# Performance work log

Hardware: AMD Instinct MI355X
Metric: run time of the kernel (lower is better)

The kernel has to match this reference:

```python
import jax, jax.numpy as jnp
import numpy as np

B, N, CT, CS, CP, H, NB = 1, 1024, 768, 384, 16, 16, 4
DH = CT // H
NL, NK = 8, 32          # n_local_tokens, n_keys
K = NL + NK
SCALE = 1.0 / np.sqrt(DH)


def _ln(x, g=None, b=None, eps=1e-5):
    m = jnp.mean(x, -1, keepdims=True)
    v = jnp.var(x, -1, keepdims=True)
    y = (x - m) * jax.lax.rsqrt(v + eps)
    if g is not None:
        y = y * g
    if b is not None:
        y = y + b
    return y


def _adaln(a, s, sln_g, sw, sb, shw):
    # AF3 AdaLN: a <- sigmoid(Lin(s_n)) * LN(a) + LinNoBias(s_n)
    an = _ln(a)
    sn = _ln(s, sln_g)
    return jax.nn.sigmoid(sn @ sw + sb) * an + sn @ shw


def _indices(X_L):
    # n_local sequence neighbours (clamped window) + n_keys spatial nearest
    off = jnp.arange(NL) - NL // 2
    loc = jnp.clip(jnp.arange(N)[:, None] + off[None, :], 0, N - 1)  # [N,NL]
    d2 = jnp.sum((X_L[:, :, None, :] - X_L[:, None, :, :]) ** 2, -1)  # [B,N,N]
    _, nk = jax.lax.top_k(-d2, NK)                                    # [B,N,NK]
    loc = jnp.broadcast_to(loc[None], (X_L.shape[0], N, NL))
    return jnp.concatenate([loc, nk], -1)                             # [B,N,K]


def setup_inputs() -> dict:
    key = jax.random.key(0)
    ks = list(jax.random.split(key, 24))
    f32 = jnp.float32

    def rn(k, shape, s=0.02):
        return (jax.random.normal(k, shape) * s).astype(f32)

    d = {}
    d['A_I'] = jax.random.normal(ks[0], (B, N, CT), f32)
    d['S_I'] = jax.random.normal(ks[1], (B, N, CS), f32)
    d['Z_II'] = jax.random.normal(ks[2], (B, N, N, CP), f32)
    d['X_L'] = jax.random.normal(ks[3], (B, N, 3), f32) * 10.0
    d['f'] = jax.random.randint(ks[4], (B, N), 0, 4)
    # attention-pair-bias block params (stacked over NB blocks)
    d['aln1_sln_g'] = jnp.ones((NB, CS), f32)
    d['aln1_sw'] = rn(ks[5], (NB, CS, CT))
    d['aln1_sb'] = jnp.zeros((NB, CT), f32)
    d['aln1_shw'] = rn(ks[6], (NB, CS, CT))
    d['Wq'] = rn(ks[7], (NB, CT, CT))
    d['bq'] = jnp.zeros((NB, CT), f32)
    d['Wk'] = rn(ks[8], (NB, CT, CT))
    d['Wv'] = rn(ks[9], (NB, CT, CT))
    d['pair_ln_g'] = jnp.ones((NB, CP), f32)
    d['pair_ln_b'] = jnp.zeros((NB, CP), f32)
    d['Wb'] = rn(ks[10], (NB, CP, H))
    d['Wg'] = rn(ks[11], (NB, CT, CT))
    d['Wo'] = rn(ks[12], (NB, CT, CT))
    d['sg_w'] = rn(ks[13], (NB, CS, CT))
    d['sg_b'] = jnp.full((NB, CT), -2.0, f32)   # LinearBiasInit(-2.0)
    # conditioned transition block params
    d['aln2_sln_g'] = jnp.ones((NB, CS), f32)
    d['aln2_sw'] = rn(ks[14], (NB, CS, CT))
    d['aln2_sb'] = jnp.zeros((NB, CT), f32)
    d['aln2_shw'] = rn(ks[15], (NB, CS, CT))
    d['t_w1'] = rn(ks[16], (NB, CT, 2 * CT))
    d['t_w2'] = rn(ks[17], (NB, CT, 2 * CT))
    d['t_w3'] = rn(ks[18], (NB, 2 * CT, CT))
    d['tsg_w'] = rn(ks[19], (NB, CS, CT))
    d['tsg_b'] = jnp.full((NB, CT), -2.0, f32)
    return d


def reference(A_I, S_I, Z_II, X_L, f,
              aln1_sln_g, aln1_sw, aln1_sb, aln1_shw,
              Wq, bq, Wk, Wv, pair_ln_g, pair_ln_b, Wb, Wg, Wo, sg_w, sg_b,
              aln2_sln_g, aln2_sw, aln2_sb, aln2_shw,
              t_w1, t_w2, t_w3, tsg_w, tsg_b):
    idx = _indices(X_L)                       # [B,N,K] int
    bb = jnp.arange(B)[:, None, None]
    nn_ = jnp.arange(N)[None, :, None]
    zg = Z_II[bb, nn_, idx]                   # [B,N,K,CP] gathered pair reps
    A = A_I
    for i in range(NB):
        # LocalAttentionPairBias
        an = _adaln(A, S_I, aln1_sln_g[i], aln1_sw[i], aln1_sb[i], aln1_shw[i])
        q = (an @ Wq[i] + bq[i]).reshape(B, N, H, DH)
        kg = (an @ Wk[i])[bb, idx].reshape(B, N, K, H, DH)
        vg = (an @ Wv[i])[bb, idx].reshape(B, N, K, H, DH)
        bias = _ln(zg, pair_ln_g[i], pair_ln_b[i]) @ Wb[i]      # [B,N,K,H]
        sc = jnp.einsum('bnhd,bnkhd->bnhk', q, kg) * SCALE + jnp.swapaxes(bias, -1, -2)
        w = jax.nn.softmax(sc, -1)                               # [B,N,H,K]
        o = jnp.einsum('bnhk,bnkhd->bnhd', w, vg).reshape(B, N, CT)
        o = jax.nn.sigmoid(an @ Wg[i]) * o                       # per-channel gate
        o = jax.nn.sigmoid(S_I @ sg_w[i] + sg_b[i]) * (o @ Wo[i])
        A = A + o                                                # dropout=0 (eval)
        # ConditionedTransitionBlock (SwiGLU, n=2)
        an2 = _adaln(A, S_I, aln2_sln_g[i], aln2_sw[i], aln2_sb[i], aln2_shw[i])
        hb = jax.nn.silu(an2 @ t_w1[i]) * (an2 @ t_w2[i])
        A = A + jax.nn.sigmoid(S_I @ tsg_w[i] + tsg_b[i]) * (hb @ t_w3[i])
    return A
```

## Files before the change

### kernel.cpp

```cpp
#include <hip/hip_runtime.h>
#include <hip/hip_bf16.h>
#include <math.h>
#include <stdint.h>

#define NTOK 1024
#define CT   768
#define CS   384
#define CP   16
#define NH   16
#define DH   48
#define NBLK 4
#define NL   8
#define NKEY 32
#define KTOT 40
#define SCALE_ 0.14433756729740643f

#define WS_BLK      8257536
#define OFF_A1SW    0
#define OFF_A1SHW   294912
#define OFF_QKVG    589824
#define OFF_WO      2949120
#define OFF_SGT     3538944
#define OFF_A2SW    4128768
#define OFF_A2SHW   4423680
#define OFF_TW1     4718592
#define OFF_TW2     5898240
#define OFF_TW3     7077888

typedef __attribute__((ext_vector_type(8))) short short8;
typedef __attribute__((ext_vector_type(4))) float f32x4;

#define AS1 __attribute__((address_space(1)))
#define AS3 __attribute__((address_space(3)))

__device__ __forceinline__ float sigmoidf_(float x) {
    return 1.0f / (1.0f + __expf(-x));
}
__device__ __forceinline__ float bf2f(unsigned short u) {
    union { unsigned int i; float f; } v; v.i = (unsigned int)u << 16; return v.f;
}
__device__ __forceinline__ unsigned short f2bf(float f) {
    return __bfloat16_as_ushort(__float2bfloat16(f));
}

__device__ __forceinline__ void gl_lds16(const void* g, void* l) {
    __builtin_amdgcn_global_load_lds((const AS1 void*)(uintptr_t)g,
                                     (AS3 void*)(uintptr_t)l, 16, 0, 0);
}

struct PrepArgs {
    const float* X_L; int* idx;
    const float* S; const float* g1; const float* g2;
    __hip_bfloat16* S_bf; __hip_bfloat16* snb;
    const float* bq; const float* sg_b; const float* tsg_b;
    float* qb; float* sb2;
};

__global__ __launch_bounds__(384)
void prep_kernel(PrepArgs pa) {
    __shared__ float ls[12];
    const int t = threadIdx.x;
    const int b = blockIdx.x;

    if (b < 256) {
        const int w = t >> 6;
        if (w >= 4) return;
        const int l = t & 63;
        const int n = b * 4 + w;
        const float* X = pa.X_L;
        int* idx = pa.idx;

        const float x0 = X[n * 3 + 0], x1 = X[n * 3 + 1], x2 = X[n * 3 + 2];
        float d[16];
        unsigned long long lkey = ~0ull;
#pragma unroll
        for (int j = 0; j < 16; ++j) {
            int m = j * 64 + l;
            float dx = x0 - X[m * 3 + 0];
            float dy = x1 - X[m * 3 + 1];
            float dz = x2 - X[m * 3 + 2];
            float v = dx * dx + dy * dy + dz * dz;
            d[j] = v;
            unsigned long long key =
                ((unsigned long long)__float_as_uint(v) << 32) | (unsigned int)m;
            lkey = key < lkey ? key : lkey;
        }
        if (l < NL) {
            int loc = n + l - NL / 2;
            loc = loc < 0 ? 0 : (loc > NTOK - 1 ? NTOK - 1 : loc);
            idx[n * KTOT + l] = loc;
        }
        for (int it = 0; it < NKEY; ++it) {
            unsigned long long rk = lkey;
#pragma unroll
            for (int s = 32; s > 0; s >>= 1) {
                unsigned long long o = __shfl_xor(rk, s, 64);
                rk = o < rk ? o : rk;
            }
            unsigned int win = (unsigned int)rk;
            if (l == 0) idx[n * KTOT + NL + it] = (int)win;
            if ((int)(win & 63) == l) {
                int jw = (int)(win >> 6);
                unsigned long long nk = ~0ull;
#pragma unroll
                for (int j = 0; j < 16; ++j) {
                    if (j == jw) d[j] = INFINITY;
                    unsigned long long key =
                        ((unsigned long long)__float_as_uint(d[j]) << 32) |
                        (unsigned int)(j * 64 + l);
                    nk = key < nk ? key : nk;
                }
                lkey = nk;
            }
        }
        return;
    }

    if (b < 1280) {
        int r = b - 256;
        int wid = t >> 6, l = t & 63;
        float v = pa.S[r * CS + t];
        float s = v;
#pragma unroll
        for (int m = 32; m > 0; m >>= 1) s += __shfl_xor(s, m, 64);
        if (l == 0) ls[wid] = s;
        __syncthreads();
        float mean = (ls[0] + ls[1] + ls[2] + ls[3] + ls[4] + ls[5]) * (1.0f / CS);
        float d = v - mean;
        float q = d * d;
#pragma unroll
        for (int m = 32; m > 0; m >>= 1) q += __shfl_xor(q, m, 64);
        if (l == 0) ls[6 + wid] = q;
        __syncthreads();
        float rstd = rsqrtf((ls[6] + ls[7] + ls[8] + ls[9] + ls[10] + ls[11]) *
                            (1.0f / CS) + 1e-5f);
        float ln = d * rstd;
        pa.S_bf[r * CS + t] = __float2bfloat16(v);
#pragma unroll
        for (int j = 0; j < 8; ++j) {
            const float* g = ((j & 1) ? pa.g2 : pa.g1) + (j >> 1) * CS;
            pa.snb[((size_t)j * NTOK + r) * CS + t] = __float2bfloat16(ln * g[t]);
        }
        return;
    }

    {
        int tt = (b - 1280) * 384 + t;
        if (tt < NBLK * 3072) {
            int i = tt / 3072, c = tt % 3072;
            pa.qb[tt] = (c < 768) ? pa.bq[i * 768 + c] : 0.0f;
        }
        if (tt < NBLK * 1536) {
            int i = tt / 1536, c = tt % 1536;
            pa.sb2[tt] = (c < 768) ? pa.sg_b[i * 768 + c] : pa.tsg_b[i * 768 + c - 768];
        }
    }
}

__global__ __launch_bounds__(256)
void adaapply_kernel(const float* __restrict__ A,
                     const __hip_bfloat16* __restrict__ SIG,
                     const __hip_bfloat16* __restrict__ SH,
                     __hip_bfloat16* __restrict__ an) {
    int r = blockIdx.x, t = threadIdx.x;
    int wid = t >> 6, l = t & 63;
    __shared__ float ls[8];
    const float* ar = A + (size_t)r * CT;
    float v0 = ar[t], v1 = ar[t + 256], v2 = ar[t + 512];
    float s = v0 + v1 + v2;
#pragma unroll
    for (int m = 32; m > 0; m >>= 1) s += __shfl_xor(s, m, 64);
    if (l == 0) ls[wid] = s;
    __syncthreads();
    float mean = (ls[0] + ls[1] + ls[2] + ls[3]) * (1.0f / CT);
    float d0 = v0 - mean, d1 = v1 - mean, d2 = v2 - mean;
    float q = d0 * d0 + d1 * d1 + d2 * d2;
#pragma unroll
    for (int m = 32; m > 0; m >>= 1) q += __shfl_xor(q, m, 64);
    if (l == 0) ls[4 + wid] = q;
    __syncthreads();
    float rstd = rsqrtf((ls[4] + ls[5] + ls[6] + ls[7]) * (1.0f / CT) + 1e-5f);
    size_t base = (size_t)r * CT;
    float dd[3] = {d0, d1, d2};
#pragma unroll
    for (int k = 0; k < 3; ++k) {
        int c = t + k * 256;
        float sg = sigmoidf_(__bfloat162float(SIG[base + c]));
        float sh = __bfloat162float(SH[base + c]);
        an[base + c] = __float2bfloat16(sg * dd[k] * rstd + sh);
    }
}

struct ConvDesc { const float* src; __hip_bfloat16* dst; int K; int N; int tstart; int srcStride; };
struct ConvTable { ConvDesc e[14]; };

__global__ __launch_bounds__(256)
void convT_kernel(ConvTable tab) {
    int b = blockIdx.x;
    int ei = 0;
#pragma unroll
    for (int j = 1; j < 14; ++j) if (b >= tab.e[j].tstart) ei = j;
    ConvDesc d = tab.e[ei];
    const float* src = d.src + (size_t)blockIdx.y * d.srcStride;
    unsigned short* dst = (unsigned short*)(d.dst + (size_t)blockIdx.y * WS_BLK);
    int tt = b - d.tstart;
    int ntn = d.N / 128;
    int k0 = (tt / ntn) * 128, n0 = (tt % ntn) * 128;

    const int ck = threadIdx.x & 15;
    const int cn = threadIdx.x >> 4;

    const float* sp = src + (size_t)(k0 + ck * 8) * d.N + n0 + cn * 8;
    f32x4 va[8], vb[8];
#pragma unroll
    for (int r = 0; r < 8; ++r) {
        va[r] = *(const f32x4*)(sp + (size_t)r * d.N);
        vb[r] = *(const f32x4*)(sp + (size_t)r * d.N + 4);
    }
    unsigned short* dp = dst + (size_t)(n0 + cn * 8) * d.K + k0 + ck * 8;
#pragma unroll
    for (int j = 0; j < 8; ++j) {
        short8 o;
#pragma unroll
        for (int e = 0; e < 8; ++e) {
            float f = (j < 4) ? va[e][j] : vb[e][j - 4];
            o[e] = (short)f2bf(f);
        }
        *(short8*)(dp + (size_t)j * d.K) = o;
    }
}

template <int MODE>
__global__ __launch_bounds__(256)
void gemmw_kernel(const __hip_bfloat16* A, const __hip_bfloat16* B1,
                  const float* cb1, const float* cb2,
                  __hip_bfloat16* outb, __hip_bfloat16* outb2,
                  int K, int N, int ldo) {
    __shared__ __align__(16) char As[2][16384];
    __shared__ __align__(16) char Bs[2][8192];

    const float* cb = cb1;
    __hip_bfloat16* outp = outb;
    if constexpr (MODE == 5) {
        int z = blockIdx.z;
        int j = z & 7, half = z >> 3;
        A += (size_t)j * NTOK * CS;
        B1 += (size_t)(j >> 1) * WS_BLK + ((j & 1) ? OFF_A2SW : OFF_A1SW)
            + (size_t)half * (OFF_A1SHW - OFF_A1SW);
        cb = half ? nullptr : (((j & 1) ? cb2 : cb1) + (j >> 1) * CT);
        outp = (half ? outb2 : outb) + (size_t)j * NTOK * CT;
    } else if constexpr (MODE == 6) {
        int z = blockIdx.z;
        B1 += (size_t)z * WS_BLK;
        cb = cb1 + z * 1536;
        outp = outb + (size_t)z * NTOK * 1536;
    }

    const int tid = threadIdx.x;
    const int lane = tid & 63;
    const int wid = tid >> 6;
    const int row0 = blockIdx.y * 128;
    const int col0 = blockIdx.x * 64;

    const int srow = tid >> 3;
    const int sg_e = (((tid & 7) ^ (srow & 7)) << 3);
    const __hip_bfloat16* ag = A + (size_t)(row0 + srow) * K + sg_e;
    const __hip_bfloat16* bg = B1 + (size_t)(col0 + srow) * K + sg_e;
    const size_t r32K = (size_t)32 * K;

    auto STAGE = [&](int bi) {
        char* al = As[bi] + tid * 16;
        char* bl = Bs[bi] + tid * 16;
        gl_lds16(ag, al);
        gl_lds16(ag + r32K, al + 4096);
        gl_lds16(ag + 2 * r32K, al + 8192);
        gl_lds16(ag + 3 * r32K, al + 12288);
        gl_lds16(bg, bl);
        gl_lds16(bg + r32K, bl + 4096);
        ag += 64; bg += 64;
    };

    f32x4 acc[2][4];
#pragma unroll
    for (int i = 0; i < 2; ++i)
#pragma unroll
        for (int j = 0; j < 4; ++j) acc[i][j] = (f32x4){0.f, 0.f, 0.f, 0.f};

    const int l15 = lane & 15;
    const int lhi = lane >> 4;
    const int nIter = K >> 6;

    STAGE(0);
    for (int it = 0; it < nIter; ++it) {
        __syncthreads();
        if (it + 1 < nIter) STAGE((it + 1) & 1);
        const char* Ab = As[it & 1];
        const char* Bb = Bs[it & 1];
#pragma unroll
        for (int kk = 0; kk < 2; ++kk) {
            const int c = lhi + 4 * kk;
            short8 a[2], bv[4];
#pragma unroll
            for (int mi = 0; mi < 2; ++mi) {
                int ra = wid * 32 + mi * 16 + l15;
                a[mi] = *(const short8*)(Ab + ra * 128 + (((c ^ (ra & 7)) << 4)));
            }
#pragma unroll
            for (int ni = 0; ni < 4; ++ni) {
                int rb = ni * 16 + l15;
                bv[ni] = *(const short8*)(Bb + rb * 128 + (((c ^ (rb & 7)) << 4)));
            }
#pragma unroll
            for (int mi = 0; mi < 2; ++mi)
#pragma unroll
                for (int ni = 0; ni < 4; ++ni)
                    acc[mi][ni] = __builtin_amdgcn_mfma_f32_16x16x32_bf16(
                        a[mi], bv[ni], acc[mi][ni], 0, 0, 0);
        }
    }

#pragma unroll
    for (int mi = 0; mi < 2; ++mi)
#pragma unroll
        for (int ni = 0; ni < 4; ++ni) {
            int col = col0 + ni * 16 + l15;
            int rbase = row0 + wid * 32 + mi * 16 + lhi * 4;
            float cbv = cb ? cb[col] : 0.0f;
            f32x4 v = acc[mi][ni];
#pragma unroll
            for (int r = 0; r < 4; ++r)
                outp[(size_t)(rbase + r) * ldo + col] = __float2bfloat16(v[r] + cbv);
        }
}

template <int MODE>
__global__ __launch_bounds__(256)
void gemm_kernel(const __hip_bfloat16* __restrict__ A,
                 const __hip_bfloat16* B1,
                 const __hip_bfloat16* B2,
                 const __hip_bfloat16* __restrict__ auxb, int ld_aux,
                 float* __restrict__ outf,
                 __hip_bfloat16* outb,
                 int K, int N, int ldo) {
    constexpr bool DUAL = (MODE == 2);
    __shared__ __align__(16) char As[2][8192];
    __shared__ __align__(16) char Bs[2][8192];
    __shared__ __align__(16) char Bs2[DUAL ? 2 : 1][DUAL ? 8192 : 16];

    const int tid = threadIdx.x;
    const int lane = tid & 63;
    const int wid = tid >> 6;
    const int wr = wid >> 1, wc = wid & 1;
    const int row0 = blockIdx.y * 64;
    const int col0 = blockIdx.x * 64;

    const int srow = tid >> 3;
    const int sg_e = (((tid & 7) ^ (srow & 7)) << 3);
    const __hip_bfloat16* ag = A + (size_t)(row0 + srow) * K + sg_e;
    const __hip_bfloat16* bg = B1 + (size_t)(col0 + srow) * K + sg_e;
    const __hip_bfloat16* bg2 = DUAL ? (B2 + (size_t)(col0 + srow) * K + sg_e) : nullptr;
    const size_t r32K = (size_t)32 * K;

    auto STAGE = [&](int bi) {
        gl_lds16(ag, As[bi] + tid * 16);
        gl_lds16(ag + r32K, As[bi] + 4096 + tid * 16);
        gl_lds16(bg, Bs[bi] + tid * 16);
        gl_lds16(bg + r32K, Bs[bi] + 4096 + tid * 16);
        if (DUAL) {
            gl_lds16(bg2, Bs2[bi] + tid * 16);
            gl_lds16(bg2 + r32K, Bs2[bi] + 4096 + tid * 16);
            bg2 += 64;
        }
        ag += 64; bg += 64;
    };

    f32x4 acc[2][2];
    f32x4 acc2[2][2];
#pragma unroll
    for (int i = 0; i < 2; ++i)
#pragma unroll
        for (int j = 0; j < 2; ++j) {
            acc[i][j] = (f32x4){0.f, 0.f, 0.f, 0.f};
            acc2[i][j] = (f32x4){0.f, 0.f, 0.f, 0.f};
        }

    const int l15 = lane & 15;
    const int lhi = lane >> 4;
    const int nIter = K >> 6;

    STAGE(0);
    for (int it = 0; it < nIter; ++it) {
        __syncthreads();
        if (it + 1 < nIter) STAGE((it + 1) & 1);
        const char* Ab = As[it & 1];
        const char* Bb = Bs[it & 1];
        const char* Cb = DUAL ? Bs2[it & 1] : nullptr;
#pragma unroll
        for (int kk = 0; kk < 2; ++kk) {
            const int c = lhi + 4 * kk;
            const int ra0 = wr * 32 + l15, ra1 = ra0 + 16;
            const int rb0 = wc * 32 + l15, rb1 = rb0 + 16;
            short8 a0 = *(const short8*)(Ab + ra0 * 128 + (((c ^ (ra0 & 7)) << 4)));
            short8 a1 = *(const short8*)(Ab + ra1 * 128 + (((c ^ (ra1 & 7)) << 4)));
            short8 b0 = *(const short8*)(Bb + rb0 * 128 + (((c ^ (rb0 & 7)) << 4)));
            short8 b1 = *(const short8*)(Bb + rb1 * 128 + (((c ^ (rb1 & 7)) << 4)));
            acc[0][0] = __builtin_amdgcn_mfma_f32_16x16x32_bf16(a0, b0, acc[0][0], 0, 0, 0);
            acc[0][1] = __builtin_amdgcn_mfma_f32_16x16x32_bf16(a0, b1, acc[0][1], 0, 0, 0);
            acc[1][0] = __builtin_amdgcn_mfma_f32_16x16x32_bf16(a1, b0, acc[1][0], 0, 0, 0);
            acc[1][1] = __builtin_amdgcn_mfma_f32_16x16x32_bf16(a1, b1, acc[1][1], 0, 0, 0);
            if (DUAL) {
                short8 c0 = *(const short8*)(Cb + rb0 * 128 + (((c ^ (rb0 & 7)) << 4)));
                short8 c1 = *(const short8*)(Cb + rb1 * 128 + (((c ^ (rb1 & 7)) << 4)));
                acc2[0][0] = __builtin_amdgcn_mfma_f32_16x16x32_bf16(a0, c0, acc2[0][0], 0, 0, 0);
                acc2[0][1] = __builtin_amdgcn_mfma_f32_16x16x32_bf16(a0, c1, acc2[0][1], 0, 0, 0);
                acc2[1][0] = __builtin_amdgcn_mfma_f32_16x16x32_bf16(a1, c0, acc2[1][0], 0, 0, 0);
                acc2[1][1] = __builtin_amdgcn_mfma_f32_16x16x32_bf16(a1, c1, acc2[1][1], 0, 0, 0);
            }
        }
    }

#pragma unroll
    for (int mi = 0; mi < 2; ++mi)
#pragma unroll
        for (int ni = 0; ni < 2; ++ni) {
            f32x4 v1 = acc[mi][ni];
            f32x4 v2 = acc2[mi][ni];
            int col = col0 + wc * 32 + ni * 16 + l15;
            int rbase = row0 + wr * 32 + mi * 16 + lhi * 4;
#pragma unroll
            for (int r = 0; r < 4; ++r) {
                int row = rbase + r;
                size_t o = (size_t)row * ldo + col;
                if (MODE == 2) {
                    float x = v1[r];
                    outb[o] = __float2bfloat16(x * sigmoidf_(x) * v2[r]);
                } else {
                    float g = sigmoidf_(__bfloat162float(auxb[(size_t)row * ld_aux + col]));
                    outf[o] += g * v1[r];
                }
            }
        }
}

__global__ __launch_bounds__(256)
void attn_kernel(const __hip_bfloat16* __restrict__ qkvg,
                 const float* __restrict__ Z,
                 const int* __restrict__ idx,
                 const float* __restrict__ pg, const float* __restrict__ pb,
                 const float* __restrict__ Wbp,
                 __hip_bfloat16* __restrict__ o2) {
    int n = blockIdx.x;
    int t = threadIdx.x;
    __shared__ __align__(16) unsigned short qs[768];
    __shared__ float sc[16][48];
    __shared__ float lnz[KTOT][16];
    __shared__ float wb[16][17];
    __shared__ float pgs[16], pbs[16];
    __shared__ int sidx[KTOT];
    __shared__ float pacc[96][8];

    wb[t >> 4][t & 15] = Wbp[t];
    if (t < 96) ((short8*)qs)[t] = ((const short8*)(qkvg + (size_t)n * 3072))[t];
    if (t >= 96 && t < 96 + KTOT) sidx[t - 96] = idx[n * KTOT + (t - 96)];
    if (t >= 160 && t < 176) pgs[t - 160] = pg[t - 160];
    if (t >= 176 && t < 192) pbs[t - 176] = pb[t - 176];
    __syncthreads();

    if (t < KTOT) {
        const f32x4* z = (const f32x4*)(Z + ((size_t)n * NTOK + sidx[t]) * CP);
        f32x4 z0 = z[0], z1 = z[1], z2 = z[2], z3 = z[3];
        float v[16];
#pragma unroll
        for (int e = 0; e < 4; ++e) { v[e] = z0[e]; v[4 + e] = z1[e]; v[8 + e] = z2[e]; v[12 + e] = z3[e]; }
        float s = 0.0f;
#pragma unroll
        for (int c = 0; c < 16; ++c) s += v[c];
        float mean = s * (1.0f / 16.0f);
        float s2 = 0.0f;
#pragma unroll
        for (int c = 0; c < 16; ++c) { float d = v[c] - mean; s2 += d * d; }
        float rstd = rsqrtf(s2 * (1.0f / 16.0f) + 1e-5f);
#pragma unroll
        for (int c = 0; c < 16; ++c) lnz[t][c] = (v[c] - mean) * rstd * pgs[c] + pbs[c];
    }
    __syncthreads();

    for (int task = t; task < NH * KTOT; task += 256) {
        int h = task / KTOT, k = task - h * KTOT;
        const short8* kp = (const short8*)((const unsigned short*)qkvg +
                                           (size_t)sidx[k] * 3072 + 768 + h * DH);
        const short8* qp = (const short8*)(qs + h * DH);
        float s = 0.0f;
#pragma unroll
        for (int j = 0; j < 6; ++j) {
            short8 kv = kp[j];
            short8 qv = qp[j];
#pragma unroll
            for (int e = 0; e < 8; ++e)
                s += bf2f((unsigned short)qv[e]) * bf2f((unsigned short)kv[e]);
        }
        float bias = 0.0f;
#pragma unroll
        for (int c = 0; c < 16; ++c) bias += lnz[k][c] * wb[c][h];
        sc[h][k] = s * SCALE_ + bias;
    }
    __syncthreads();

    {
        int h = t >> 4, l = t & 15;
        float v0 = sc[h][l];
        float v1 = sc[h][l + 16];
        float v2 = (l < 8) ? sc[h][l + 32] : -INFINITY;
        float mx = fmaxf(fmaxf(v0, v1), v2);
#pragma unroll
        for (int m = 8; m > 0; m >>= 1) mx = fmaxf(mx, __shfl_xor(mx, m, 16));
        float e0 = __expf(v0 - mx), e1 = __expf(v1 - mx);
        float e2 = (l < 8) ? __expf(v2 - mx) : 0.0f;
        float sm = e0 + e1 + e2;
#pragma unroll
        for (int m = 8; m > 0; m >>= 1) sm += __shfl_xor(sm, m, 16);
        float inv = 1.0f / sm;
        sc[h][l] = e0 * inv;
        sc[h][l + 16] = e1 * inv;
        if (l < 8) sc[h][l + 32] = e2 * inv;
    }
    __syncthreads();

    float acc[8] = {0, 0, 0, 0, 0, 0, 0, 0};
    const int half = (t >= 96) ? 1 : 0;
    const int tt = t - half * 96;
    if (t < 192) {
        int h = tt / 6, c6 = tt - h * 6;
        int d0 = c6 * 8;
        const unsigned short* vbase = (const unsigned short*)qkvg + 1536 + h * DH + d0;
        for (int k = half * 20; k < half * 20 + 20; ++k) {
            short8 vv = *(const short8*)(vbase + (size_t)sidx[k] * 3072);
            float w = sc[h][k];
#pragma unroll
            for (int e = 0; e < 8; ++e) acc[e] += w * bf2f((unsigned short)vv[e]);
        }
    }
    if (half && t < 192) {
#pragma unroll
        for (int e = 0; e < 8; ++e) pacc[tt][e] = acc[e];
    }
    __syncthreads();
    if (t < 96) {
        int h = t / 6, c6 = t - h * 6;
        int d0 = c6 * 8;
        short8 gv = *(const short8*)((const unsigned short*)qkvg +
                                     (size_t)n * 3072 + 2304 + h * DH + d0);
        short8 ov;
#pragma unroll
        for (int e = 0; e < 8; ++e) {
            float g = sigmoidf_(bf2f((unsigned short)gv[e]));
            ov[e] = (short)f2bf(g * (acc[e] + pacc[t][e]));
        }
        *(short8*)((unsigned short*)o2 + (size_t)n * CT + h * DH + d0) = ov;
    }
}

extern "C" void kernel_launch(void* const* d_in, const int* in_sizes, int n_in,
                              void* d_out, int out_size, void* d_ws, size_t ws_size,
                              hipStream_t stream) {
    const float* A_I  = (const float*)d_in[0];
    const float* S_I  = (const float*)d_in[1];
    const float* Z_II = (const float*)d_in[2];
    const float* X_L  = (const float*)d_in[3];
    const float* aln1_sln_g = (const float*)d_in[5];
    const float* aln1_sw    = (const float*)d_in[6];
    const float* aln1_sb    = (const float*)d_in[7];
    const float* aln1_shw   = (const float*)d_in[8];
    const float* Wq  = (const float*)d_in[9];
    const float* bq  = (const float*)d_in[10];
    const float* Wk  = (const float*)d_in[11];
    const float* Wv  = (const float*)d_in[12];
    const float* pair_ln_g = (const float*)d_in[13];
    const float* pair_ln_b = (const float*)d_in[14];
    const float* Wbp = (const float*)d_in[15];
    const float* Wg  = (const float*)d_in[16];
    const float* Wo  = (const float*)d_in[17];
    const float* sg_w = (const float*)d_in[18];
    const float* sg_b = (const float*)d_in[19];
    const float* aln2_sln_g = (const float*)d_in[20];
    const float* aln2_sw    = (const float*)d_in[21];
    const float* aln2_sb    = (const float*)d_in[22];
    const float* aln2_shw   = (const float*)d_in[23];
    const float* t_w1 = (const float*)d_in[24];
    const float* t_w2 = (const float*)d_in[25];
    const float* t_w3 = (const float*)d_in[26];
    const float* tsg_w = (const float*)d_in[27];
    const float* tsg_b = (const float*)d_in[28];
    (void)in_sizes; (void)n_in; (void)out_size; (void)ws_size;

    float* A = (float*)d_out;

    char* ws = (char*)d_ws;
    size_t off = 0;
    auto alloc = [&](size_t bytes) {
        void* p = ws + off;
        off += (bytes + 255) & ~(size_t)255;
        return p;
    };
    int*   idx    = (int*)  alloc(NTOK * KTOT * 4);
    __hip_bfloat16* S_bf  = (__hip_bfloat16*)alloc((size_t)NTOK * CS * 2);
    __hip_bfloat16* snb   = (__hip_bfloat16*)alloc((size_t)8 * NTOK * CS * 2);
    __hip_bfloat16* an    = (__hip_bfloat16*)alloc((size_t)NTOK * CT * 2);
    __hip_bfloat16* qkvg  = (__hip_bfloat16*)alloc((size_t)NTOK * 3072 * 2);
    __hip_bfloat16* sgateb= (__hip_bfloat16*)alloc((size_t)NBLK * NTOK * 1536 * 2);
    __hip_bfloat16* SIG   = (__hip_bfloat16*)alloc((size_t)8 * NTOK * CT * 2);
    __hip_bfloat16* SH    = (__hip_bfloat16*)alloc((size_t)8 * NTOK * CT * 2);
    __hip_bfloat16* o2    = (__hip_bfloat16*)alloc((size_t)NTOK * CT * 2);
    __hip_bfloat16* hb    = (__hip_bfloat16*)alloc((size_t)NTOK * 2 * CT * 2);
    float* qkvgbias = (float*)alloc((size_t)NBLK * 3072 * 4);
    float* sgbias   = (float*)alloc((size_t)NBLK * 1536 * 4);
    __hip_bfloat16* Wbuf = (__hip_bfloat16*)alloc((size_t)NBLK * WS_BLK * 2);

    hipMemcpyAsync(A, A_I, (size_t)NTOK * CT * 4, hipMemcpyDeviceToDevice, stream);

    {
        PrepArgs pa;
        pa.X_L = X_L; pa.idx = idx;
        pa.S = S_I; pa.g1 = aln1_sln_g; pa.g2 = aln2_sln_g;
        pa.S_bf = S_bf; pa.snb = snb;
        pa.bq = bq; pa.sg_b = sg_b; pa.tsg_b = tsg_b;
        pa.qb = qkvgbias; pa.sb2 = sgbias;
        prep_kernel<<<1312, 384, 0, stream>>>(pa);
    }

    {
        ConvTable tab;
        int p = 0, ts = 0;
        auto add = [&](const float* s, size_t dstOff, int Kk, int Nn, int sstride) {
            tab.e[p].src = s; tab.e[p].dst = Wbuf + dstOff; tab.e[p].K = Kk;
            tab.e[p].N = Nn; tab.e[p].tstart = ts; tab.e[p].srcStride = sstride;
            ts += (Kk / 128) * (Nn / 128); ++p;
        };
        add(aln1_sw,  OFF_A1SW,           384, 768,  CS * CT);
        add(aln1_shw, OFF_A1SHW,          384, 768,  CS * CT);
        add(Wq, OFF_QKVG + 0 * 589824,    768, 768,  CT * CT);
        add(Wk, OFF_QKVG + 1 * 589824,    768, 768,  CT * CT);
        add(Wv, OFF_QKVG + 2 * 589824,    768, 768,  CT * CT);
        add(Wg, OFF_QKVG + 3 * 589824,    768, 768,  CT * CT);
        add(Wo, OFF_WO,                   768, 768,  CT * CT);
        add(sg_w,  OFF_SGT,               384, 768,  CS * CT);
        add(tsg_w, OFF_SGT + 768 * 384,   384, 768,  CS * CT);
        add(aln2_sw,  OFF_A2SW,           384, 768,  CS * CT);
        add(aln2_shw, OFF_A2SHW,          384, 768,  CS * CT);
        add(t_w1, OFF_TW1,                768, 1536, CT * 2 * CT);
        add(t_w2, OFF_TW2,                768, 1536, CT * 2 * CT);
        add(t_w3, OFF_TW3,                1536, 768, 2 * CT * CT);
        convT_kernel<<<dim3(ts, NBLK), 256, 0, stream>>>(tab);
    }

    gemmw_kernel<5><<<dim3(12, 8, 16), 256, 0, stream>>>(
        snb, Wbuf, aln1_sb, aln2_sb, SIG, SH, 384, 768, 768);
    gemmw_kernel<6><<<dim3(24, 8, 4), 256, 0, stream>>>(
        S_bf, Wbuf + OFF_SGT, sgbias, nullptr, sgateb, nullptr, 384, 1536, 1536);

    for (int i = 0; i < NBLK; ++i) {
        const __hip_bfloat16* Wb_i = Wbuf + (size_t)i * WS_BLK;
        __hip_bfloat16* sg_i = sgateb + (size_t)i * NTOK * 1536;

        adaapply_kernel<<<NTOK, 256, 0, stream>>>(
            A, SIG + (size_t)(2 * i) * NTOK * CT, SH + (size_t)(2 * i) * NTOK * CT, an);
        gemmw_kernel<4><<<dim3(48, 8), 256, 0, stream>>>(
            an, Wb_i + OFF_QKVG, qkvgbias + (size_t)i * 3072, nullptr,
            qkvg, nullptr, 768, 3072, 3072);
        attn_kernel<<<NTOK, 256, 0, stream>>>(
            qkvg, Z_II, idx, pair_ln_g + (size_t)i * CP, pair_ln_b + (size_t)i * CP,
            Wbp + (size_t)i * CP * NH, o2);
        gemm_kernel<3><<<dim3(12, 16), 256, 0, stream>>>(
            o2, Wb_i + OFF_WO, nullptr, sg_i, 1536, A, nullptr, 768, 768, 768);

        adaapply_kernel<<<NTOK, 256, 0, stream>>>(
            A, SIG + (size_t)(2 * i + 1) * NTOK * CT, SH + (size_t)(2 * i + 1) * NTOK * CT, an);
        gemm_kernel<2><<<dim3(24, 16), 256, 0, stream>>>(
            an, Wb_i + OFF_TW1, Wb_i + OFF_TW2, nullptr, 0, nullptr, hb, 768, 1536, 1536);
        gemm_kernel<3><<<dim3(12, 16), 256, 0, stream>>>(
            hb, Wb_i + OFF_TW3, nullptr, sg_i + 768, 1536, A, nullptr, 1536, 768, 768);
    }
}
```

Measured before the change: 407.7 us.

## Merge prep and weight conversion, fuse hoisted GEMMs, split-K residual GEMMs with atomics

Folds the weight-transpose/convert work into the prep kernel as extra blocks and shrinks prep to 256 threads. The two hoisted conditioning GEMMs become one launch, saving launches and tail idle time. The residual-adding GEMMs (Wo and t_w3) now split K across two z-slices and accumulate into A with atomicAdd, doubling block count for these small 12x16 grids. In exchange this adds atomic traffic, makes the floating-point summation order nondeterministic, and leaves odd leftover labels in the code.

After: 378.1 us. 7.3% less time.

```diff
diff --git a/kernel.cpp b/kernel.cpp
--- a/kernel.cpp
+++ b/kernel.cpp
@@ -27,6 +27,9 @@
 #define OFF_TW2     5898240
 #define OFF_TW3     7077888
 
+#define NCONVT 504
+#define NPREPB 1328
+
 typedef __attribute__((ext_vector_type(8))) short short8;
 typedef __attribute__((ext_vector_type(4))) float f32x4;
 
@@ -48,7 +51,9 @@
                                      (AS3 void*)(uintptr_t)l, 16, 0, 0);
 }
 
-struct PrepArgs {
+struct ConvDesc { const float* src; __hip_bfloat16* dst; int K; int N; int tstart; int srcStride; };
+struct ConvPrep {
+    ConvDesc e[14];
     const float* X_L; int* idx;
     const float* S; const float* g1; const float* g2;
     __hip_bfloat16* S_bf; __hip_bfloat16* snb;
@@ -56,15 +61,51 @@
     float* qb; float* sb2;
 };
 
-__global__ __launch_bounds__(384)
-void prep_kernel(PrepArgs pa) {
-    __shared__ float ls[12];
+__global__ __launch_bounds__(256)
+void convprep_kernel(ConvPrep pa) {
+    __shared__ float ls[8];
     const int t = threadIdx.x;
     const int b = blockIdx.x;
 
+    if (b >= NPREPB) {
+        int cb = b - NPREPB;
+        int wblk = cb / NCONVT;
+        int tt_all = cb % NCONVT;
+        int ei = 0;
+#pragma unroll
+        for (int j = 1; j < 14; ++j) if (tt_all >= pa.e[j].tstart) ei = j;
+        ConvDesc d = pa.e[ei];
+        const float* src = d.src + (size_t)wblk * d.srcStride;
+        unsigned short* dst = (unsigned short*)(d.dst + (size_t)wblk * WS_BLK);
+        int tt = tt_all - d.tstart;
+        int ntn = d.N / 128;
+        int k0 = (tt / ntn) * 128, n0 = (tt % ntn) * 128;
+
+        const int ck = t & 15;
+        const int cn = t >> 4;
+        const float* sp = src + (size_t)(k0 + ck * 8) * d.N + n0 + cn * 8;
+        f32x4 va[8], vb[8];
+#pragma unroll
+        for (int r = 0; r < 8; ++r) {
+            va[r] = *(const f32x4*)(sp + (size_t)r * d.N);
+            vb[r] = *(const f32x4*)(sp + (size_t)r * d.N + 4);
+        }
+        unsigned short* dp = dst + (size_t)(n0 + cn * 8) * d.K + k0 + ck * 8;
+#pragma unroll
+        for (int j = 0; j < 8; ++j) {
+            short8 o;
+#pragma unroll
+            for (int e = 0; e < 8; ++e) {
+                float f = (j < 4) ? va[e][j] : vb[e][j - 4];
+                o[e] = (short)f2bf(f);
+            }
+            *(short8*)(dp + (size_t)j * d.K) = o;
+        }
+        return;
+    }
+
     if (b < 256) {
         const int w = t >> 6;
-        if (w >= 4) return;
         const int l = t & 63;
         const int n = b * 4 + w;
         const float* X = pa.X_L;
@@ -119,33 +160,37 @@
     if (b < 1280) {
         int r = b - 256;
         int wid = t >> 6, l = t & 63;
-        float v = pa.S[r * CS + t];
-        float s = v;
+        const float* S = pa.S;
+        float v0 = S[r * CS + t];
+        float v1 = (t < 128) ? S[r * CS + 256 + t] : 0.0f;
+        float s = v0 + v1;
 #pragma unroll
         for (int m = 32; m > 0; m >>= 1) s += __shfl_xor(s, m, 64);
         if (l == 0) ls[wid] = s;
         __syncthreads();
-        float mean = (ls[0] + ls[1] + ls[2] + ls[3] + ls[4] + ls[5]) * (1.0f / CS);
-        float d = v - mean;
-        float q = d * d;
+        float mean = (ls[0] + ls[1] + ls[2] + ls[3]) * (1.0f / CS);
+        float d0 = v0 - mean, d1 = v1 - mean;
+        float q = d0 * d0 + ((t < 128) ? d1 * d1 : 0.0f);
 #pragma unroll
         for (int m = 32; m > 0; m >>= 1) q += __shfl_xor(q, m, 64);
-        if (l == 0) ls[6 + wid] = q;
+        if (l == 0) ls[4 + wid] = q;
         __syncthreads();
-        float rstd = rsqrtf((ls[6] + ls[7] + ls[8] + ls[9] + ls[10] + ls[11]) *
-                            (1.0f / CS) + 1e-5f);
-        float ln = d * rstd;
-        pa.S_bf[r * CS + t] = __float2bfloat16(v);
+        float rstd = rsqrtf((ls[4] + ls[5] + ls[6] + ls[7]) * (1.0f / CS) + 1e-5f);
+        float ln0 = d0 * rstd, ln1 = d1 * rstd;
+        pa.S_bf[r * CS + t] = __float2bfloat16(v0);
+        if (t < 128) pa.S_bf[r * CS + 256 + t] = __float2bfloat16(v1);
 #pragma unroll
         for (int j = 0; j < 8; ++j) {
             const float* g = ((j & 1) ? pa.g2 : pa.g1) + (j >> 1) * CS;
-            pa.snb[((size_t)j * NTOK + r) * CS + t] = __float2bfloat16(ln * g[t]);
+            size_t base = ((size_t)j * NTOK + r) * CS;
+            pa.snb[base + t] = __float2bfloat16(ln0 * g[t]);
+            if (t < 128) pa.snb[base + 256 + t] = __float2bfloat16(ln1 * g[256 + t]);
         }
         return;
     }
 
     {
-        int tt = (b - 1280) * 384 + t;
+        int tt = (b - 1280) * 256 + t;
         if (tt < NBLK * 3072) {
             int i = tt / 3072, c = tt % 3072;
             pa.qb[tt] = (c < 768) ? pa.bq[i * 768 + c] : 0.0f;
@@ -191,70 +236,201 @@
     }
 }
 
-struct ConvDesc { const float* src; __hip_bfloat16* dst; int K; int N; int tstart; int srcStride; };
-struct ConvTable { ConvDesc e[14]; };
+struct HoistArgs {
+    const __hip_bfloat16* snb; const __hip_bfloat16* S_bf;
+    const __hip_bfloat16* Wbuf;
+    const float* a1sb; const float* a2sb; const float* sgbias;
+    __hip_bfloat16* SIG; __hip_bfloat16* SH; __hip_bfloat16* sgateb;
+};
 
 __global__ __launch_bounds__(256)
-void convT_kernel(ConvTable tab) {
-    int b = blockIdx.x;
-    int ei = 0;
-#pragma unroll
-    for (int j = 1; j < 14; ++j) if (b >= tab.e[j].tstart) ei = j;
-    ConvDesc d = tab.e[ei];
-    const float* src = d.src + (size_t)blockIdx.y * d.srcStride;
-    unsigned short* dst = (unsigned short*)(d.dst + (size_t)blockIdx.y * WS_BLK);
-    int tt = b - d.tstart;
-    int ntn = d.N / 128;
-    int k0 = (tt / ntn) * 128, n0 = (tt % ntn) * 128;
-
-    const int ck = threadIdx.x & 15;
-    const int cn = threadIdx.x >> 4;
-
-    const float* sp = src + (size_t)(k0 + ck * 8) * d.N + n0 + cn * 8;
-    f32x4 va[8], vb[8];
-#pragma unroll
-    for (int r = 0; r < 8; ++r) {
-        va[r] = *(const f32x4*)(sp + (size_t)r * d.N);
-        vb[r] = *(const f32x4*)(sp + (size_t)r * d.N + 4);
-    }
-    unsigned short* dp = dst + (size_t)(n0 + cn * 8) * d.K + k0 + ck * 8;
-#pragma unroll
-    for (int j = 0; j < 8; ++j) {
-        short8 o;
-#pragma unroll
-        for (int e = 0; e < 8; ++e) {
-            float f = (j < 4) ? va[e][j] : vb[e][j - 4];
-            o[e] = (short)f2bf(f);
-        }
-        *(short8*)(dp + (size_t)j * d.K) = o;
-    }
-}
-
-template <int MODE>
+void gemmh_kernel(HoistArgs ha) {
+    __shared__ __align__(16) char As[2][16384];
+    __shared__ __align__(16) char Bs[2][8192];
+
+    const __hip_bfloat16* A;
+    const __hip_bfloat16* B1;
+    const float* cb;
+    __hip_bfloat16* outp;
+    int ldo;
+    {
+        int b = blockIdx.x;
+        if (b < 1536) {
+            int z = b / 96, rem = b % 96;
+            int y = rem / 12, x = rem % 12;
+            int j = z & 7, half = z >> 3;
+            A = ha.snb + (size_t)j * NTOK * CS;
+            B1 = ha.Wbuf + (size_t)(j >> 1) * WS_BLK
+               + ((j & 1) ? OFF_A2SW : OFF_A1SW)
+               + (size_t)half * (OFF_A1SHW - OFF_A1SW);
+            cb = half ? nullptr : (((j & 1) ? ha.a2sb : ha.a1sb) + (j >> 1) * CT);
+            outp = (half ? ha.SH : ha.SIG) + (size_t)j * NTOK * CT;
+            ldo = 768;
+            outp += 0;
+            A += 0;
+            blockIdx_x_decl:;
+            {
+                const int row0 = y * 128, col0 = x * 64;
+                goto body_entry_0;
+                body_entry_0:;
+                ((void)0);
+                const int tid = threadIdx.x;
+                const int lane = tid & 63;
+                const int wid = tid >> 6;
+                const int srow = tid >> 3;
+                const int sg_e = (((tid & 7) ^ (srow & 7)) << 3);
+                const __hip_bfloat16* ag = A + (size_t)(row0 + srow) * CS + sg_e;
+                const __hip_bfloat16* bg = B1 + (size_t)(col0 + srow) * CS + sg_e;
+                const size_t r32K = (size_t)32 * CS;
+                f32x4 acc[2][4];
+#pragma unroll
+                for (int i = 0; i < 2; ++i)
+#pragma unroll
+                    for (int jj = 0; jj < 4; ++jj) acc[i][jj] = (f32x4){0.f, 0.f, 0.f, 0.f};
+                const int l15 = lane & 15;
+                const int lhi = lane >> 4;
+                const int nIter = CS >> 6;
+                auto STAGE = [&](int bi) {
+                    char* al = As[bi] + tid * 16;
+                    char* bl = Bs[bi] + tid * 16;
+                    gl_lds16(ag, al);
+                    gl_lds16(ag + r32K, al + 4096);
+                    gl_lds16(ag + 2 * r32K, al + 8192);
+                    gl_lds16(ag + 3 * r32K, al + 12288);
+                    gl_lds16(bg, bl);
+                    gl_lds16(bg + r32K, bl + 4096);
+                    ag += 64; bg += 64;
+                };
+                STAGE(0);
+                for (int it = 0; it < nIter; ++it) {
+                    __syncthreads();
+                    if (it + 1 < nIter) STAGE((it + 1) & 1);
+                    const char* Ab = As[it & 1];
+                    const char* Bb = Bs[it & 1];
+#pragma unroll
+                    for (int kk = 0; kk < 2; ++kk) {
+                        const int c = lhi + 4 * kk;
+                        short8 a[2], bv[4];
+#pragma unroll
+                        for (int mi = 0; mi < 2; ++mi) {
+                            int ra = wid * 32 + mi * 16 + l15;
+                            a[mi] = *(const short8*)(Ab + ra * 128 + (((c ^ (ra & 7)) << 4)));
+                        }
+#pragma unroll
+                        for (int ni = 0; ni < 4; ++ni) {
+                            int rb = ni * 16 + l15;
+                            bv[ni] = *(const short8*)(Bb + rb * 128 + (((c ^ (rb & 7)) << 4)));
+                        }
+#pragma unroll
+                        for (int mi = 0; mi < 2; ++mi)
+#pragma unroll
+                            for (int ni = 0; ni < 4; ++ni)
+                                acc[mi][ni] = __builtin_amdgcn_mfma_f32_16x16x32_bf16(
+                                    a[mi], bv[ni], acc[mi][ni], 0, 0, 0);
+                    }
+                }
+#pragma unroll
+                for (int mi = 0; mi < 2; ++mi)
+#pragma unroll
+                    for (int ni = 0; ni < 4; ++ni) {
+                        int col = col0 + ni * 16 + l15;
+                        int rbase = row0 + wid * 32 + mi * 16 + lhi * 4;
+                        float cbv = cb ? cb[col] : 0.0f;
+                        f32x4 v = acc[mi][ni];
+#pragma unroll
+                        for (int r = 0; r < 4; ++r)
+                            outp[(size_t)(rbase + r) * ldo + col] = __float2bfloat16(v[r] + cbv);
+                    }
+                return;
+            }
+        } else {
+            int b2 = b - 1536;
+            int z = b2 / 192, rem = b2 % 192;
+            int y = rem / 24, x = rem % 24;
+            A = ha.S_bf;
+            B1 = ha.Wbuf + OFF_SGT + (size_t)z * WS_BLK;
+            cb = ha.sgbias + z * 1536;
+            outp = ha.sgateb + (size_t)z * NTOK * 1536;
+            ldo = 1536;
+            const int row0 = y * 128, col0 = x * 64;
+            const int tid = threadIdx.x;
+            const int lane = tid & 63;
+            const int wid = tid >> 6;
+            const int srow = tid >> 3;
+            const int sg_e = (((tid & 7) ^ (srow & 7)) << 3);
+            const __hip_bfloat16* ag = A + (size_t)(row0 + srow) * CS + sg_e;
+            const __hip_bfloat16* bg = B1 + (size_t)(col0 + srow) * CS + sg_e;
+            const size_t r32K = (size_t)32 * CS;
+            f32x4 acc[2][4];
+#pragma unroll
+            for (int i = 0; i < 2; ++i)
+#pragma unroll
+                for (int jj = 0; jj < 4; ++jj) acc[i][jj] = (f32x4){0.f, 0.f, 0.f, 0.f};
+            const int l15 = lane & 15;
+            const int lhi = lane >> 4;
+            const int nIter = CS >> 6;
+            auto STAGE = [&](int bi) {
+                char* al = As[bi] + tid * 16;
+                char* bl = Bs[bi] + tid * 16;
+                gl_lds16(ag, al);
+                gl_lds16(ag + r32K, al + 4096);
+                gl_lds16(ag + 2 * r32K, al + 8192);
+                gl_lds16(ag + 3 * r32K, al + 12288);
+                gl_lds16(bg, bl);
+                gl_lds16(bg + r32K, bl + 4096);
+                ag += 64; bg += 64;
+            };
+            STAGE(0);
+            for (int it = 0; it < nIter; ++it) {
+                __syncthreads();
+                if (it + 1 < nIter) STAGE((it + 1) & 1);
+                const char* Ab = As[it & 1];
+                const char* Bb = Bs[it & 1];
+#pragma unroll
+                for (int kk = 0; kk < 2; ++kk) {
+                    const int c = lhi + 4 * kk;
+                    short8 a[2], bv[4];
+#pragma unroll
+                    for (int mi = 0; mi < 2; ++mi) {
+                        int ra = wid * 32 + mi * 16 + l15;
+                        a[mi] = *(const short8*)(Ab + ra * 128 + (((c ^ (ra & 7)) << 4)));
+                    }
+#pragma unroll
+                    for (int ni = 0; ni < 4; ++ni) {
+                        int rb = ni * 16 + l15;
+                        bv[ni] = *(const short8*)(Bb + rb * 128 + (((c ^ (rb & 7)) << 4)));
+                    }
+#pragma unroll
+                    for (int mi = 0; mi < 2; ++mi)
+#pragma unroll
+                        for (int ni = 0; ni < 4; ++ni)
+                            acc[mi][ni] = __builtin_amdgcn_mfma_f32_16x16x32_bf16(
+                                a[mi], bv[ni], acc[mi][ni], 0, 0, 0);
+                }
+            }
+#pragma unroll
+            for (int mi = 0; mi < 2; ++mi)
+#pragma unroll
+                for (int ni = 0; ni < 4; ++ni) {
+                    int col = col0 + ni * 16 + l15;
+                    int rbase = row0 + wid * 32 + mi * 16 + lhi * 4;
+                    float cbv = cb ? cb[col] : 0.0f;
+                    f32x4 v = acc[mi][ni];
+#pragma unroll
+                    for (int r = 0; r < 4; ++r)
+                        outp[(size_t)(rbase + r) * ldo + col] = __float2bfloat16(v[r] + cbv);
+                }
+            return;
+        }
+    }
+}
+
 __global__ __launch_bounds__(256)
 void gemmw_kernel(const __hip_bfloat16* A, const __hip_bfloat16* B1,
-                  const float* cb1, const float* cb2,
-                  __hip_bfloat16* outb, __hip_bfloat16* outb2,
+                  const float* cb, __hip_bfloat16* outb,
                   int K, int N, int ldo) {
     __shared__ __align__(16) char As[2][16384];
     __shared__ __align__(16) char Bs[2][8192];
-
-    const float* cb = cb1;
-    __hip_bfloat16* outp = outb;
-    if constexpr (MODE == 5) {
-        int z = blockIdx.z;
-        int j = z & 7, half = z >> 3;
-        A += (size_t)j * NTOK * CS;
-        B1 += (size_t)(j >> 1) * WS_BLK + ((j & 1) ? OFF_A2SW : OFF_A1SW)
-            + (size_t)half * (OFF_A1SHW - OFF_A1SW);
-        cb = half ? nullptr : (((j & 1) ? cb2 : cb1) + (j >> 1) * CT);
-        outp = (half ? outb2 : outb) + (size_t)j * NTOK * CT;
-    } else if constexpr (MODE == 6) {
-        int z = blockIdx.z;
-        B1 += (size_t)z * WS_BLK;
-        cb = cb1 + z * 1536;
-        outp = outb + (size_t)z * NTOK * 1536;
-    }
 
     const int tid = threadIdx.x;
     const int lane = tid & 63;
@@ -329,7 +505,8 @@
             f32x4 v = acc[mi][ni];
 #pragma unroll
             for (int r = 0; r < 4; ++r)
-                outp[(size_t)(rbase + r) * ldo + col] = __float2bfloat16(v[r] + cbv);
+                outp_store:
+                outb[(size_t)(rbase + r) * ldo + col] = __float2bfloat16(v[r] + cbv);
         }
 }
 
@@ -341,7 +518,7 @@
                  const __hip_bfloat16* __restrict__ auxb, int ld_aux,
                  float* __restrict__ outf,
                  __hip_bfloat16* outb,
-                 int K, int N, int ldo) {
+                 int Kfull, int Ksub, int N, int ldo) {
     constexpr bool DUAL = (MODE == 2);
     __shared__ __align__(16) char As[2][8192];
     __shared__ __align__(16) char Bs[2][8192];
@@ -353,13 +530,14 @@
     const int wr = wid >> 1, wc = wid & 1;
     const int row0 = blockIdx.y * 64;
     const int col0 = blockIdx.x * 64;
+    const int koff = blockIdx.z * Ksub;
 
     const int srow = tid >> 3;
     const int sg_e = (((tid & 7) ^ (srow & 7)) << 3);
-    const __hip_bfloat16* ag = A + (size_t)(row0 + srow) * K + sg_e;
-    const __hip_bfloat16* bg = B1 + (size_t)(col0 + srow) * K + sg_e;
-    const __hip_bfloat16* bg2 = DUAL ? (B2 + (size_t)(col0 + srow) * K + sg_e) : nullptr;
-    const size_t r32K = (size_t)32 * K;
+    const __hip_bfloat16* ag = A + (size_t)(row0 + srow) * Kfull + koff + sg_e;
+    const __hip_bfloat16* bg = B1 + (size_t)(col0 + srow) * Kfull + koff + sg_e;
+    const __hip_bfloat16* bg2 = DUAL ? (B2 + (size_t)(col0 + srow) * Kfull + koff + sg_e) : nullptr;
+    const size_t r32K = (size_t)32 * Kfull;
 
     auto STAGE = [&](int bi) {
         gl_lds16(ag, As[bi] + tid * 16);
@@ -386,7 +564,7 @@
 
     const int l15 = lane & 15;
     const int lhi = lane >> 4;
-    const int nIter = K >> 6;
+    const int nIter = Ksub >> 6;
 
     STAGE(0);
     for (int it = 0; it < nIter; ++it) {
@@ -436,7 +614,7 @@
                     outb[o] = __float2bfloat16(x * sigmoidf_(x) * v2[r]);
                 } else {
                     float g = sigmoidf_(__bfloat162float(auxb[(size_t)row * ld_aux + col]));
-                    outf[o] += g * v1[r];
+                    atomicAdd(&outf[o], g * v1[r]);
                 }
             }
         }
@@ -619,21 +797,11 @@
     hipMemcpyAsync(A, A_I, (size_t)NTOK * CT * 4, hipMemcpyDeviceToDevice, stream);
 
     {
-        PrepArgs pa;
-        pa.X_L = X_L; pa.idx = idx;
-        pa.S = S_I; pa.g1 = aln1_sln_g; pa.g2 = aln2_sln_g;
-        pa.S_bf = S_bf; pa.snb = snb;
-        pa.bq = bq; pa.sg_b = sg_b; pa.tsg_b = tsg_b;
-        pa.qb = qkvgbias; pa.sb2 = sgbias;
-        prep_kernel<<<1312, 384, 0, stream>>>(pa);
-    }
-
-    {
-        ConvTable tab;
+        ConvPrep pa;
         int p = 0, ts = 0;
         auto add = [&](const float* s, size_t dstOff, int Kk, int Nn, int sstride) {
-            tab.e[p].src = s; tab.e[p].dst = Wbuf + dstOff; tab.e[p].K = Kk;
-            tab.e[p].N = Nn; tab.e[p].tstart = ts; tab.e[p].srcStride = sstride;
+            pa.e[p].src = s; pa.e[p].dst = Wbuf + dstOff; pa.e[p].K = Kk;
+            pa.e[p].N = Nn; pa.e[p].tstart = ts; pa.e[p].srcStride = sstride;
             ts += (Kk / 128) * (Nn / 128); ++p;
         };
         add(aln1_sw,  OFF_A1SW,           384, 768,  CS * CT);
@@ -650,13 +818,21 @@
         add(t_w1, OFF_TW1,                768, 1536, CT * 2 * CT);
         add(t_w2, OFF_TW2,                768, 1536, CT * 2 * CT);
         add(t_w3, OFF_TW3,                1536, 768, 2 * CT * CT);
-        convT_kernel<<<dim3(ts, NBLK), 256, 0, stream>>>(tab);
-    }
-
-    gemmw_kernel<5><<<dim3(12, 8, 16), 256, 0, stream>>>(
-        snb, Wbuf, aln1_sb, aln2_sb, SIG, SH, 384, 768, 768);
-    gemmw_kernel<6><<<dim3(24, 8, 4), 256, 0, stream>>>(
-        S_bf, Wbuf + OFF_SGT, sgbias, nullptr, sgateb, nullptr, 384, 1536, 1536);
+        pa.X_L = X_L; pa.idx = idx;
+        pa.S = S_I; pa.g1 = aln1_sln_g; pa.g2 = aln2_sln_g;
+        pa.S_bf = S_bf; pa.snb = snb;
+        pa.bq = bq; pa.sg_b = sg_b; pa.tsg_b = tsg_b;
+        pa.qb = qkvgbias; pa.sb2 = sgbias;
+        convprep_kernel<<<NPREPB + ts * NBLK, 256, 0, stream>>>(pa);
+    }
+
+    {
+        HoistArgs ha;
+        ha.snb = snb; ha.S_bf = S_bf; ha.Wbuf = Wbuf;
+        ha.a1sb = aln1_sb; ha.a2sb = aln2_sb; ha.sgbias = sgbias;
+        ha.SIG = SIG; ha.SH = SH; ha.sgateb = sgateb;
+        gemmh_kernel<<<1536 + 768, 256, 0, stream>>>(ha);
+    }
 
     for (int i = 0; i < NBLK; ++i) {
         const __hip_bfloat16* Wb_i = Wbuf + (size_t)i * WS_BLK;
@@ -664,20 +840,19 @@
 
         adaapply_kernel<<<NTOK, 256, 0, stream>>>(
             A, SIG + (size_t)(2 * i) * NTOK * CT, SH + (size_t)(2 * i) * NTOK * CT, an);
-        gemmw_kernel<4><<<dim3(48, 8), 256, 0, stream>>>(
-            an, Wb_i + OFF_QKVG, qkvgbias + (size_t)i * 3072, nullptr,
-            qkvg, nullptr, 768, 3072, 3072);
+        gemmw_kernel<<<dim3(48, 8), 256, 0, stream>>>(
+            an, Wb_i + OFF_QKVG, qkvgbias + (size_t)i * 3072, qkvg, 768, 3072, 3072);
         attn_kernel<<<NTOK, 256, 0, stream>>>(
             qkvg, Z_II, idx, pair_ln_g + (size_t)i * CP, pair_ln_b + (size_t)i * CP,
             Wbp + (size_t)i * CP * NH, o2);
-        gemm_kernel<3><<<dim3(12, 16), 256, 0, stream>>>(
-            o2, Wb_i + OFF_WO, nullptr, sg_i, 1536, A, nullptr, 768, 768, 768);
+        gemm_kernel<3><<<dim3(12, 16, 2), 256, 0, stream>>>(
+            o2, Wb_i + OFF_WO, nullptr, sg_i, 1536, A, nullptr, 768, 384, 768, 768);
 
         adaapply_kernel<<<NTOK, 256, 0, stream>>>(
             A, SIG + (size_t)(2 * i + 1) * NTOK * CT, SH + (size_t)(2 * i + 1) * NTOK * CT, an);
-        gemm_kernel<2><<<dim3(24, 16), 256, 0, stream>>>(
-            an, Wb_i + OFF_TW1, Wb_i + OFF_TW2, nullptr, 0, nullptr, hb, 768, 1536, 1536);
-        gemm_kernel<3><<<dim3(12, 16), 256, 0, stream>>>(
-            hb, Wb_i + OFF_TW3, nullptr, sg_i + 768, 1536, A, nullptr, 1536, 768, 768);
-    }
-}
+        gemm_kernel<2><<<dim3(24, 16, 1), 256, 0, stream>>>(
+            an, Wb_i + OFF_TW1, Wb_i + OFF_TW2, nullptr, 0, nullptr, hb, 768, 768, 1536, 1536);
+        gemm_kernel<3><<<dim3(12, 16, 2), 256, 0, stream>>>(
+            hb, Wb_i + OFF_TW3, nullptr, sg_i + 768, 1536, A, nullptr, 1536, 768, 768, 768);
+    }
+}
```
